# Optimization experiments

Hardware: AMD Instinct MI355X
Metric: run time of the kernel (lower is better)

## Reference

```python
import jax, jax.numpy as jnp
import numpy as np

DIM = 512
HEADS = 8
DHEAD = 64
WIN = 128
QK_SCALE = 8.0
LN_EPS = 1e-5


def setup_inputs() -> dict:
    key = jax.random.key(0)
    ks = jax.random.split(key, 5)
    B, N = 8, 4096
    x = jax.random.normal(ks[0], (B, N, DIM), jnp.float32)
    w_qkv = jax.random.normal(ks[1], (3 * HEADS * DHEAD, DIM), jnp.float32) * 0.02
    w_out = jax.random.normal(ks[2], (DIM, HEADS * DHEAD), jnp.float32) * 0.02
    b_out = jnp.zeros((DIM,), jnp.float32)
    w_ff1 = jax.random.normal(ks[3], (4 * DIM, DIM), jnp.float32) * 0.02
    w_ff2 = jax.random.normal(ks[4], (DIM, 4 * DIM), jnp.float32) * 0.02
    return {
        'x': x, 'w_qkv': w_qkv,
        'q_scale': jnp.ones((DHEAD,), jnp.float32),
        'k_scale': jnp.ones((DHEAD,), jnp.float32),
        'w_out': w_out, 'b_out': b_out,
        'ln1_g': jnp.ones((DIM,), jnp.float32), 'ln1_b': jnp.zeros((DIM,), jnp.float32),
        'ff_ln_g': jnp.ones((DIM,), jnp.float32), 'ff_ln_b': jnp.zeros((DIM,), jnp.float32),
        'w_ff1': w_ff1, 'w_ff2': w_ff2,
    }


def _ln(x, g, b):
    m = jnp.mean(x, axis=-1, keepdims=True)
    v = jnp.mean((x - m) ** 2, axis=-1, keepdims=True)
    return (x - m) * jax.lax.rsqrt(v + LN_EPS) * g + b


def _l2norm(t):
    return t / jnp.clip(jnp.linalg.norm(t, axis=-1, keepdims=True), 1e-12)


def _rotary(t, pos):
    # t: (B, H, N, DHEAD); standard (non-xpos) rotary, half-split style
    inv_freq = 1.0 / (10000.0 ** (jnp.arange(0, DHEAD, 2, dtype=jnp.float32) / DHEAD))
    freqs = pos[:, None] * inv_freq                      # (N, DHEAD/2)
    emb = jnp.concatenate([freqs, freqs], axis=-1)       # (N, DHEAD)
    cos, sin = jnp.cos(emb), jnp.sin(emb)
    t1, t2 = t[..., : DHEAD // 2], t[..., DHEAD // 2:]
    rot = jnp.concatenate([-t2, t1], axis=-1)
    return t * cos + rot * sin


def reference(x, w_qkv, q_scale, k_scale, w_out, b_out, ln1_g, ln1_b,
              ff_ln_g, ff_ln_b, w_ff1, w_ff2):
    B, N, D = x.shape
    nw = N // WIN

    # ---- LocalMHA (prenorm, qk-rmsnorm, sliding window, causal) ----
    h = _ln(x, ln1_g, ln1_b)
    qkv = h @ w_qkv.T                                    # (B, N, 3*H*DHEAD)
    q, k, v = jnp.split(qkv, 3, axis=-1)

    def to_heads(t):
        return t.reshape(B, N, HEADS, DHEAD).transpose(0, 2, 1, 3)  # (B,H,N,d)

    q, k, v = to_heads(q), to_heads(k), to_heads(v)
    q = _l2norm(q) * q_scale
    k = _l2norm(k) * k_scale
    pos = jnp.arange(N, dtype=jnp.float32)
    q = _rotary(q, pos)
    k = _rotary(k, pos)

    # bucket into windows; keys/values look back one window
    bq = q.reshape(B, HEADS, nw, WIN, DHEAD)
    bk = k.reshape(B, HEADS, nw, WIN, DHEAD)
    bv = v.reshape(B, HEADS, nw, WIN, DHEAD)

    def look_back(t):
        prev = jnp.concatenate([jnp.zeros_like(t[:, :, :1]), t[:, :, :-1]], axis=2)
        return jnp.concatenate([prev, t], axis=3)

    kk, vv = look_back(bk), look_back(bv)

    qpos = jnp.arange(N, dtype=jnp.int32).reshape(nw, WIN)
    kprev = jnp.concatenate([jnp.full((1, WIN), -1, jnp.int32), qpos[:-1]], axis=0)
    kpos = jnp.concatenate([kprev, qpos], axis=1)
    mask = (qpos[:, :, None] >= kpos[:, None, :]) & (kpos[:, None, :] >= 0)

    sim = jnp.einsum('bhnid,bhnjd->bhnij', bq, kk) * QK_SCALE
    sim = jnp.where(mask, sim, -1e9)
    attn = jax.nn.softmax(sim, axis=-1)
    out = jnp.einsum('bhnij,bhnjd->bhnid', attn, vv)
    out = out.reshape(B, HEADS, N, DHEAD).transpose(0, 2, 1, 3).reshape(B, N, HEADS * DHEAD)
    x = x + out @ w_out.T + b_out

    # ---- FeedForward: LN -> Linear(4D, no bias) -> GELU -> Linear(D, no bias) ----
    hf = _ln(x, ff_ln_g, ff_ln_b)
    ff = jax.nn.gelu(hf @ w_ff1.T, approximate=False) @ w_ff2.T
    return x + ff
```

## Files before the change

kernel.cpp:

```cpp
#include <hip/hip_runtime.h>
#include <cstdint>
#include <cstddef>

typedef __bf16 bf16;
typedef __bf16 bf16x8 __attribute__((ext_vector_type(8)));
typedef float f32x4 __attribute__((ext_vector_type(4)));

#define DEV static __device__ __forceinline__

constexpr int BATCH = 8;
constexpr int SEQ = 4096;
constexpr int DIM = 512;
constexpr int HEADS = 8;
constexpr int DH = 64;
constexpr int WIN = 128;
constexpr int NW = SEQ / WIN;
constexpr int TOK = BATCH * SEQ;
constexpr float EPS = 1e-5f;

constexpr size_t R_EL   = (size_t)TOK * DIM;
constexpr size_t C_QKV  = 0;
constexpr size_t C_WOUT = 786432;
constexpr size_t C_WF1  = 1048576;
constexpr size_t C_WF2  = 2097152;
constexpr size_t C_SM   = 3145728;
constexpr size_t P_EL   = 3148416;

DEV void gload_lds16(const void* g, void* l) {
  __builtin_amdgcn_global_load_lds((__attribute__((address_space(1))) void*)g,
                                   (__attribute__((address_space(3))) void*)l,
                                   16, 0, 0);
}

DEV f32x4 mfma16(bf16x8 a, bf16x8 b, f32x4 c) {
  return __builtin_amdgcn_mfma_f32_16x16x32_bf16(a, b, c, 0, 0, 0);
}

DEV float fast_gelu(float v) {
  const float z = fabsf(v) * 0.7071067811865476f;
  const float t = __builtin_amdgcn_rcpf(1.0f + 0.3275911f * z);
  const float p = t * (0.254829592f +
                  t * (-0.284496736f +
                  t * (1.421413741f +
                  t * (-1.453152027f +
                  t * 1.061405429f))));
  const float e = __expf(-z * z);
  const float erfa = 1.0f - p * e;
  const float cdf = 0.5f + copysignf(0.5f * erfa, v);
  return v * cdf;
}

struct SrcPtrs { const void* p[12]; };

DEV void copy8(const void* src, long si, bf16* dst, bool f32) {
  if (f32) {
    const float4* s = (const float4*)((const float*)src + si);
    float4 a = s[0], b = s[1];
    bf16x8 o;
    o[0] = (bf16)a.x; o[1] = (bf16)a.y; o[2] = (bf16)a.z; o[3] = (bf16)a.w;
    o[4] = (bf16)b.x; o[5] = (bf16)b.y; o[6] = (bf16)b.z; o[7] = (bf16)b.w;
    *(bf16x8*)dst = o;
  } else {
    *(bf16x8*)dst = *(const bf16x8*)((const bf16*)src + si);
  }
}

__global__ __launch_bounds__(256) void ingest_kernel(SrcPtrs sp, bf16* cano) {
  const bool f32 = (((const unsigned short*)sp.p[2])[0] == 0);
  const long e = (long)threadIdx.x * 8;
  int b = blockIdx.x;
  if (b < 384)  { long o = (long)b * 2048 + e; copy8(sp.p[1], o, cano + C_QKV + o, f32); return; }
  b -= 384;
  if (b < 128)  { long o = (long)b * 2048 + e; copy8(sp.p[4], o, cano + C_WOUT + o, f32); return; }
  b -= 128;
  if (b < 512)  { long o = (long)b * 2048 + e; copy8(sp.p[10], o, cano + C_WF1 + o, f32); return; }
  b -= 512;
  if (b < 512)  { long o = (long)b * 2048 + e; copy8(sp.p[11], o, cano + C_WF2 + o, f32); return; }
  b -= 512;
  const long o = (long)b * 2048 + e;
  if (o >= 2688) return;
  const void* src; long si;
  if      (o < 64)   { src = sp.p[2]; si = o; }
  else if (o < 128)  { src = sp.p[3]; si = o - 64; }
  else if (o < 640)  { src = sp.p[5]; si = o - 128; }
  else if (o < 1152) { src = sp.p[6]; si = o - 640; }
  else if (o < 1664) { src = sp.p[7]; si = o - 1152; }
  else if (o < 2176) { src = sp.p[8]; si = o - 1664; }
  else               { src = sp.p[9]; si = o - 2176; }
  copy8(src, si, cano + C_SM + o, f32);
}

__global__ __launch_bounds__(256) void ln_kernel(const void* __restrict__ in,
                                                 const bf16* __restrict__ gg,
                                                 const bf16* __restrict__ bb,
                                                 bf16* __restrict__ out,
                                                 const unsigned short* __restrict__ probe,
                                                 int raw) {
  const int wave = threadIdx.x >> 6, lane = threadIdx.x & 63;
  const int row = blockIdx.x * 4 + wave;
  const size_t base = (size_t)row * DIM + lane * 8;
  float f[8];
  if (raw && probe[0] == 0) {
    const float4* p = (const float4*)((const float*)in + base);
    float4 a = p[0], bq = p[1];
    f[0] = a.x; f[1] = a.y; f[2] = a.z; f[3] = a.w;
    f[4] = bq.x; f[5] = bq.y; f[6] = bq.z; f[7] = bq.w;
  } else {
    bf16x8 v = *(const bf16x8*)((const bf16*)in + base);
#pragma unroll
    for (int i = 0; i < 8; ++i) f[i] = (float)v[i];
  }
  float s = 0.f, sq = 0.f;
#pragma unroll
  for (int i = 0; i < 8; ++i) { s += f[i]; sq += f[i] * f[i]; }
#pragma unroll
  for (int m = 32; m; m >>= 1) { s += __shfl_xor(s, m); sq += __shfl_xor(sq, m); }
  const float mean = s * (1.0f / DIM);
  const float var = fmaxf(sq * (1.0f / DIM) - mean * mean, 0.0f);
  const float rs = rsqrtf(var + EPS);
  bf16x8 gv = *(const bf16x8*)(gg + lane * 8);
  bf16x8 bv = *(const bf16x8*)(bb + lane * 8);
  bf16x8 o;
#pragma unroll
  for (int i = 0; i < 8; ++i) o[i] = (bf16)((f[i] - mean) * rs * (float)gv[i] + (float)bv[i]);
  *(bf16x8*)((bf16*)out + base) = o;
}

template <int MODE>
__global__ __launch_bounds__(512) void gemm_bt(const bf16* __restrict__ A,
                                               const bf16* __restrict__ Bw,
                                               bf16* __restrict__ O0, bf16* __restrict__ O1,
                                               bf16* __restrict__ O2,
                                               float* __restrict__ Of,
                                               const void* __restrict__ Xraw,
                                               const bf16* __restrict__ Xb,
                                               const bf16* __restrict__ bias,
                                               const unsigned short* __restrict__ probe,
                                               int K, int bstride, int ostride, int gx) {
  extern __shared__ __align__(16) bf16 smem[];
  const int tid = threadIdx.x;
  const int wid = tid >> 6, lane = tid & 63;
  const int l15 = lane & 15, quad = lane >> 4;
  const int id = blockIdx.x;
  const int per = gx * 8;
  const int tM = ((id / per) * 8 + (id & 7)) * 256;
  const int tN = ((id % per) >> 3) * 128;
  const int wM = (wid >> 1) * 64, wN = (wid & 1) * 64;
  const int kq = (quad ^ ((l15 >> 1) & 3)) * 8;
  f32x4 acc[4][4];
  const f32x4 z = {0.f, 0.f, 0.f, 0.f};
#pragma unroll
  for (int i = 0; i < 4; ++i)
#pragma unroll
    for (int j = 0; j < 4; ++j) acc[i][j] = z;

  const int cA0 = tid,       rA0 = cA0 >> 2, sA0 = (((cA0 & 3) ^ ((cA0 >> 3) & 3)) * 8);
  const int cA1 = tid + 512, rA1 = cA1 >> 2, sA1 = (((cA1 & 3) ^ ((cA1 >> 3) & 3)) * 8);
  const int cB0 = tid,       rB0 = cB0 >> 2, sB0 = sA0;

  auto stage = [&](int t, int p) {
    const int k0 = t * 32;
    bf16* dA = smem + p * 12288;
    bf16* dB = dA + 8192;
    gload_lds16(A  + (size_t)(tM + rA0) * K       + k0 + sA0, &dA[cA0 * 8]);
    gload_lds16(A  + (size_t)(tM + rA1) * K       + k0 + sA1, &dA[cA1 * 8]);
    gload_lds16(Bw + (size_t)(tN + rB0) * bstride + k0 + sB0, &dB[cB0 * 8]);
  };

  const int nt = K >> 5;
  stage(0, 0);
  stage(1, 1);
  __builtin_amdgcn_sched_barrier(0);
  asm volatile("s_waitcnt vmcnt(3)" ::: "memory");
  __builtin_amdgcn_s_barrier();
  __builtin_amdgcn_sched_barrier(0);

  int cur = 0;
  for (int t = 0; t < nt; ++t) {
    if (t + 2 < nt) {
      int nx = cur + 2; if (nx >= 3) nx -= 3;
      stage(t + 2, nx);
    }
    const bf16* As = smem + cur * 12288;
    const bf16* Bs = As + 8192;
    bf16x8 aF[4], bF[4];
#pragma unroll
    for (int i = 0; i < 4; ++i) aF[i] = *(const bf16x8*)&As[(wM + i * 16 + l15) * 32 + kq];
#pragma unroll
    for (int j = 0; j < 4; ++j) bF[j] = *(const bf16x8*)&Bs[(wN + j * 16 + l15) * 32 + kq];
#pragma unroll
    for (int i = 0; i < 4; ++i)
#pragma unroll
      for (int j = 0; j < 4; ++j) acc[i][j] = mfma16(aF[i], bF[j], acc[i][j]);
    if (t < nt - 1) {
      __builtin_amdgcn_sched_barrier(0);
      if (t + 2 < nt) asm volatile("s_waitcnt vmcnt(3)" ::: "memory");
      else            asm volatile("s_waitcnt vmcnt(0)" ::: "memory");
      __builtin_amdgcn_s_barrier();
      __builtin_amdgcn_sched_barrier(0);
    }
    ++cur; if (cur == 3) cur = 0;
  }
  const int q0 = nt % 3;
  bf16* eb = smem + q0 * 12288;

  if constexpr (MODE == 0) {
    bf16* ob = eb + wid * 1152;
    const int colbase = tN + wN;
    const int which = colbase >> 9;
    const int head = (colbase >> 6) & 7;
    bf16* dst = which == 0 ? O0 : (which == 1 ? O1 : O2);
    const int ch = lane & 7;
    float scv[8], invf[8];
    if (which < 2) {
      const bf16* sc = which ? bias : Xb;
      bf16x8 s8 = *(const bf16x8*)(sc + ch * 8);
#pragma unroll
      for (int u = 0; u < 8; ++u) {
        scv[u] = (float)s8[u] * (which == 0 ? 8.0f : 1.0f);
        invf[u] = exp2f(-(float)((ch & 3) * 8 + u) * (13.287712379549449f / 32.0f));
      }
    }
#pragma unroll
    for (int i = 0; i < 4; ++i) {
#pragma unroll
      for (int j = 0; j < 4; ++j)
#pragma unroll
        for (int r = 0; r < 4; ++r)
          ob[(quad * 4 + r) * 72 + j * 16 + l15] = (bf16)acc[i][j][r];
#pragma unroll
      for (int t = 0; t < 2; ++t) {
        const int rr = t * 8 + (lane >> 3);
        const int rowg = tM + wM + i * 16 + rr;
        bf16x8 ov = *(const bf16x8*)&ob[rr * 72 + ch * 8];
        float f[8];
#pragma unroll
        for (int u = 0; u < 8; ++u) f[u] = (float)ov[u];
        if (which < 2) {
          float ss = 0.f;
#pragma unroll
          for (int u = 0; u < 8; ++u) ss += f[u] * f[u];
          ss += __shfl_xor(ss, 1); ss += __shfl_xor(ss, 2); ss += __shfl_xor(ss, 4);
          const float rs = 1.0f / fmaxf(sqrtf(ss), 1e-12f);
#pragma unroll
          for (int u = 0; u < 8; ++u) f[u] *= rs * scv[u];
          float pf[8];
#pragma unroll
          for (int u = 0; u < 8; ++u) pf[u] = __shfl_xor(f[u], 4);
          const float pos = (float)(rowg & (SEQ - 1));
#pragma unroll
          for (int u = 0; u < 8; ++u) {
            float sn, cs;
            __sincosf(pos * invf[u], &sn, &cs);
            const float rot = (ch < 4) ? -pf[u] : pf[u];
            f[u] = f[u] * cs + rot * sn;
          }
        }
        bf16x8 o8;
#pragma unroll
        for (int u = 0; u < 8; ++u) o8[u] = (bf16)f[u];
        const int bb = rowg >> 12, n = rowg & (SEQ - 1);
        *(bf16x8*)(dst + ((size_t)(bb * HEADS + head) * SEQ + n) * DH + ch * 8) = o8;
      }
    }
    return;
  }

  if constexpr (MODE == 1) {
    bf16* ob = eb + wid * 1152;
    const int ch = lane & 7;
    bf16x8 bias8 = *(const bf16x8*)(bias + tN + wN + ch * 8);
    const bool xf32 = (probe[0] == 0);
#pragma unroll
    for (int i = 0; i < 4; ++i) {
#pragma unroll
      for (int j = 0; j < 4; ++j)
#pragma unroll
        for (int r = 0; r < 4; ++r)
          ob[(quad * 4 + r) * 72 + j * 16 + l15] = (bf16)acc[i][j][r];
#pragma unroll
      for (int t = 0; t < 2; ++t) {
        const int rr = t * 8 + (lane >> 3);
        const int rowg = tM + wM + i * 16 + rr;
        bf16x8 ov = *(const bf16x8*)&ob[rr * 72 + ch * 8];
        bf16x8 o8;
        const size_t idx = (size_t)rowg * DIM + tN + wN + ch * 8;
        float xr[8];
        if (xf32) {
          const float4* xp = (const float4*)((const float*)Xraw + idx);
          float4 a = xp[0], bq = xp[1];
          xr[0] = a.x; xr[1] = a.y; xr[2] = a.z; xr[3] = a.w;
          xr[4] = bq.x; xr[5] = bq.y; xr[6] = bq.z; xr[7] = bq.w;
        } else {
          bf16x8 xv = *(const bf16x8*)((const bf16*)Xraw + idx);
#pragma unroll
          for (int u = 0; u < 8; ++u) xr[u] = (float)xv[u];
        }
#pragma unroll
        for (int u = 0; u < 8; ++u) o8[u] = (bf16)((float)ov[u] + xr[u] + (float)bias8[u]);
        *(bf16x8*)(O0 + idx) = o8;
      }
    }
    return;
  }
}

__global__ __launch_bounds__(512, 2) void ffn_fused(const bf16* __restrict__ hf,
                                                    const bf16* __restrict__ W1,
                                                    const bf16* __restrict__ W2,
                                                    const bf16* __restrict__ x2,
                                                    float* __restrict__ out) {
  extern __shared__ __align__(16) bf16 smem[];
  const int tid = threadIdx.x;
  const int wid = tid >> 6, lane = tid & 63;
  const int l15 = lane & 15, quad = lane >> 4;
  const int tM = blockIdx.x * 128;
  const int wM  = (wid >> 2) * 64;
  const int wN1 = (wid & 3) * 32;
  const int wN2 = (wid & 3) * 128;
  const int kq = (quad ^ ((l15 >> 1) & 3)) * 8;
  bf16* f1c = smem + 24576;

  const int srow = tid >> 2;
  const int scol = ((tid & 3) ^ ((tid >> 3) & 3)) * 8;

  auto stage1 = [&](int cc, int t, int p) {
    const int k0 = t * 32;
    bf16* dH = smem + p * 8192;
    bf16* dW = dH + 4096;
    gload_lds16(hf + (size_t)(tM + srow) * DIM + k0 + scol, &dH[tid * 8]);
    gload_lds16(W1 + (size_t)(cc * 128 + srow) * DIM + k0 + scol, &dW[tid * 8]);
  };

  f32x4 acc2[4][8];
  const f32x4 z = {0.f, 0.f, 0.f, 0.f};
#pragma unroll
  for (int i = 0; i < 4; ++i)
#pragma unroll
    for (int j = 0; j < 8; ++j) acc2[i][j] = z;

  stage1(0, 0, 0);
  stage1(0, 1, 1);
  __builtin_amdgcn_sched_barrier(0);
  asm volatile("s_waitcnt vmcnt(2)" ::: "memory");
  __builtin_amdgcn_s_barrier();
  __builtin_amdgcn_sched_barrier(0);

  for (int c = 0; c < 16; ++c) {
    f32x4 acc1[4][2];
#pragma unroll
    for (int i = 0; i < 4; ++i) { acc1[i][0] = z; acc1[i][1] = z; }
    int cur = 0;
    for (int t = 0; t < 16; ++t) {
      if (t + 2 < 16) {
        int nx = cur + 2; if (nx >= 3) nx -= 3;
        stage1(c, t + 2, nx);
      }
      const bf16* Hs = smem + cur * 8192;
      const bf16* Ws = Hs + 4096;
      bf16x8 aF[4], bF[2];
#pragma unroll
      for (int i = 0; i < 4; ++i) aF[i] = *(const bf16x8*)&Hs[(wM + i * 16 + l15) * 32 + kq];
#pragma unroll
      for (int j = 0; j < 2; ++j) bF[j] = *(const bf16x8*)&Ws[(wN1 + j * 16 + l15) * 32 + kq];
#pragma unroll
      for (int i = 0; i < 4; ++i)
#pragma unroll
        for (int j = 0; j < 2; ++j) acc1[i][j] = mfma16(aF[i], bF[j], acc1[i][j]);
      if (t < 15) {
        __builtin_amdgcn_sched_barrier(0);
        if (t + 2 < 16) asm volatile("s_waitcnt vmcnt(2)" ::: "memory");
        else            asm volatile("s_waitcnt vmcnt(0)" ::: "memory");
        __builtin_amdgcn_s_barrier();
        __builtin_amdgcn_sched_barrier(0);
      }
      ++cur; if (cur == 3) cur = 0;
    }
    __builtin_amdgcn_sched_barrier(0);
    __builtin_amdgcn_s_barrier();
    __builtin_amdgcn_sched_barrier(0);
#pragma unroll
    for (int i = 0; i < 4; ++i)
#pragma unroll
      for (int j = 0; j < 2; ++j)
#pragma unroll
        for (int r = 0; r < 4; ++r) {
          const int rowW = wM + i * 16 + quad * 4 + r;
          const int colW = wN1 + j * 16 + l15;
          f1c[rowW * 128 + ((((colW >> 3) ^ (rowW & 7))) << 3) + (colW & 7)] =
              (bf16)fast_gelu(acc1[i][j][r]);
        }
    if (c < 15) { stage1(c + 1, 0, 0); stage1(c + 1, 1, 1); }
    asm volatile("s_waitcnt lgkmcnt(0)" ::: "memory");
    __builtin_amdgcn_sched_barrier(0);
    __builtin_amdgcn_s_barrier();
    __builtin_amdgcn_sched_barrier(0);
    const bf16* w2c = W2 + c * 128;
#pragma unroll
    for (int kk = 0; kk < 4; ++kk) {
      bf16x8 a2[4], b2[8];
#pragma unroll
      for (int i = 0; i < 4; ++i) {
        const int row = wM + i * 16 + l15;
        a2[i] = *(const bf16x8*)&f1c[row * 128 + (((kk * 4 + quad) ^ (l15 & 7)) << 3)];
      }
#pragma unroll
      for (int j = 0; j < 8; ++j)
        b2[j] = *(const bf16x8*)(w2c + (size_t)(wN2 + j * 16 + l15) * 2048 + kk * 32 + quad * 8);
#pragma unroll
      for (int i = 0; i < 4; ++i)
#pragma unroll
        for (int j = 0; j < 8; ++j) acc2[i][j] = mfma16(a2[i], b2[j], acc2[i][j]);
    }
    if (c < 15) {
      __builtin_amdgcn_sched_barrier(0);
      asm volatile("s_waitcnt vmcnt(2)" ::: "memory");
      __builtin_amdgcn_s_barrier();
      __builtin_amdgcn_sched_barrier(0);
    }
  }

  __builtin_amdgcn_sched_barrier(0);
  __builtin_amdgcn_s_barrier();
  __builtin_amdgcn_sched_barrier(0);
  float* obf = (float*)f1c + wid * 1024;
  const int ch = lane & 7;
#pragma unroll
  for (int i = 0; i < 4; ++i)
#pragma unroll
    for (int jh = 0; jh < 2; ++jh) {
#pragma unroll
      for (int j2 = 0; j2 < 4; ++j2)
#pragma unroll
        for (int r = 0; r < 4; ++r)
          obf[(quad * 4 + r) * 64 + j2 * 16 + l15] = acc2[i][jh * 4 + j2][r];
#pragma unroll
      for (int t = 0; t < 2; ++t) {
        const int rr = t * 8 + (lane >> 3);
        const int rowg = tM + wM + i * 16 + rr;
        const size_t idx = (size_t)rowg * DIM + wN2 + jh * 64 + ch * 8;
        const float4* rp = (const float4*)&obf[rr * 64 + ch * 8];
        float4 a = rp[0], b = rp[1];
        float f[8] = {a.x, a.y, a.z, a.w, b.x, b.y, b.z, b.w};
        bf16x8 xv = *(const bf16x8*)(x2 + idx);
#pragma unroll
        for (int u = 0; u < 8; ++u) f[u] += (float)xv[u];
        float4 o0 = {f[0], f[1], f[2], f[3]}, o1 = {f[4], f[5], f[6], f[7]};
        ((float4*)(out + idx))[0] = o0;
        ((float4*)(out + idx))[1] = o1;
      }
    }
}

__global__ __launch_bounds__(256, 3) void attn_kernel(const bf16* __restrict__ q,
                                                      const bf16* __restrict__ k,
                                                      const bf16* __restrict__ v,
                                                      bf16* __restrict__ ao) {
  __shared__ __align__(16) bf16 kv[256 * 72];
  __shared__ __align__(16) bf16 pbuf[4][16 * 136];
  const int w = blockIdx.x, h = blockIdx.y, b = blockIdx.z;
  const int tid = threadIdx.x;
  const int wv = tid >> 6, lane = tid & 63;
  const int l15 = lane & 15, quad = lane >> 4;
  const size_t bh = (size_t)b * HEADS + h;
  const bf16* qb = q + bh * SEQ * DH;
  const bf16* kb = k + bh * SEQ * DH;
  const bf16* vb = v + bh * SEQ * DH;
  const int t0 = (w - 1) * WIN;

#pragma unroll
  for (int it = 0; it < 8; ++it) {
    const int c = it * 256 + tid;
    const int tok = c >> 3, ch = c & 7;
    int gt = t0 + tok; gt = gt < 0 ? 0 : gt;
    *(bf16x8*)&kv[tok * 72 + ch * 8] = *(const bf16x8*)(kb + (size_t)gt * DH + ch * 8);
  }
  bf16x8 aQ[2][2];
#pragma unroll
  for (int qt = 0; qt < 2; ++qt) {
    const int qtok = w * WIN + wv * 32 + qt * 16 + l15;
#pragma unroll
    for (int ks = 0; ks < 2; ++ks)
      aQ[qt][ks] = *(const bf16x8*)(qb + (size_t)qtok * DH + ks * 32 + quad * 8);
  }
  int gtv = t0 + tid; gtv = gtv < 0 ? 0 : gtv;
  bf16x8 vld[8];
#pragma unroll
  for (int dg = 0; dg < 8; ++dg)
    vld[dg] = *(const bf16x8*)(vb + (size_t)gtv * DH + dg * 8);
  __syncthreads();

  bf16x8 aP[2][8];
#pragma unroll
  for (int qt = 0; qt < 2; ++qt) {
    f32x4 sreg[16];
#pragma unroll
    for (int nt = 0; nt < 16; ++nt) {
      f32x4 a = {0.f, 0.f, 0.f, 0.f};
#pragma unroll
      for (int ks = 0; ks < 2; ++ks) {
        bf16x8 bK = *(const bf16x8*)&kv[(nt * 16 + l15) * 72 + ks * 32 + quad * 8];
        a = mfma16(aQ[qt][ks], bK, a);
      }
      sreg[nt] = a;
    }
    const int qlb = wv * 32 + qt * 16 + quad * 4;
    float rinv[4];
#pragma unroll
    for (int r = 0; r < 4; ++r) {
      const int ql = qlb + r;
      float sum = 0.f;
#pragma unroll
      for (int nt = 0; nt < 16; ++nt) {
        const int j = nt * 16 + l15;
        const bool valid = (nt < 8) ? (w > 0) : (ql >= j - WIN);
        const float p = valid ? __expf(sreg[nt][r]) : 0.0f;
        sreg[nt][r] = p;
        sum += p;
      }
#pragma unroll
      for (int m = 8; m; m >>= 1) sum += __shfl_xor(sum, m);
      rinv[r] = 1.0f / sum;
    }
#pragma unroll
    for (int half = 0; half < 2; ++half) {
#pragma unroll
      for (int ntw = 0; ntw < 8; ++ntw)
#pragma unroll
        for (int r = 0; r < 4; ++r)
          pbuf[wv][(quad * 4 + r) * 136 + ntw * 16 + l15] =
              (bf16)(sreg[half * 8 + ntw][r] * rinv[r]);
#pragma unroll
      for (int kk = 0; kk < 4; ++kk)
        aP[qt][half * 4 + kk] = *(const bf16x8*)&pbuf[wv][l15 * 136 + kk * 32 + quad * 8];
    }
  }
  __syncthreads();

#pragma unroll
  for (int dg = 0; dg < 8; ++dg)
#pragma unroll
    for (int i = 0; i < 8; ++i)
      kv[(dg * 8 + i) * 264 + tid] = vld[dg][i];
  __syncthreads();

#pragma unroll
  for (int qt = 0; qt < 2; ++qt) {
#pragma unroll
    for (int dt = 0; dt < 4; ++dt) {
      f32x4 o = {0.f, 0.f, 0.f, 0.f};
#pragma unroll
      for (int ks2 = 0; ks2 < 8; ++ks2) {
        bf16x8 bV = *(const bf16x8*)&kv[(dt * 16 + l15) * 264 + ks2 * 32 + quad * 8];
        o = mfma16(aP[qt][ks2], bV, o);
      }
#pragma unroll
      for (int r = 0; r < 4; ++r)
        pbuf[wv][(quad * 4 + r) * 136 + dt * 16 + l15] = (bf16)o[r];
    }
#pragma unroll
    for (int t = 0; t < 2; ++t) {
      const int rr = t * 8 + (lane >> 3), ch = lane & 7;
      bf16x8 ov = *(const bf16x8*)&pbuf[wv][rr * 136 + ch * 8];
      const int tok = w * WIN + wv * 32 + qt * 16 + rr;
      *(bf16x8*)(ao + ((size_t)b * SEQ + tok) * DIM + h * DH + ch * 8) = ov;
    }
  }
}

extern "C" void kernel_launch(void* const* d_in, const int* in_sizes, int n_in,
                              void* d_out, int out_size, void* d_ws, size_t ws_size,
                              hipStream_t stream) {
  (void)in_sizes; (void)n_in; (void)out_size; (void)ws_size;
  float* out = (float*)d_out;
  bf16* cano = (bf16*)d_ws;
  const unsigned short* probe = (const unsigned short*)d_in[2];

  SrcPtrs sp;
  for (int i = 0; i < 12; ++i) sp.p[i] = d_in[i];

  bf16* slot0 = cano + P_EL;
  bf16* slot1 = cano + P_EL + R_EL;
  bf16* slot2 = cano + P_EL + 2 * R_EL;
  bf16* slot3 = cano + P_EL + 3 * R_EL;

  const bf16* qsc  = cano + C_SM + 0;
  const bf16* ksc  = cano + C_SM + 64;
  const bf16* bout = cano + C_SM + 128;
  const bf16* l1g  = cano + C_SM + 640;
  const bf16* l1b  = cano + C_SM + 1152;
  const bf16* lfg  = cano + C_SM + 1664;
  const bf16* lfb  = cano + C_SM + 2176;

  constexpr int LDSB = 3 * 12288 * 2;
  constexpr int LDSF = 81920;
  static bool attr_done = false;
  if (!attr_done) {
    hipFuncSetAttribute((const void*)gemm_bt<0>, hipFuncAttributeMaxDynamicSharedMemorySize, LDSB);
    hipFuncSetAttribute((const void*)gemm_bt<1>, hipFuncAttributeMaxDynamicSharedMemorySize, LDSB);
    hipFuncSetAttribute((const void*)ffn_fused, hipFuncAttributeMaxDynamicSharedMemorySize, LDSF);
    attr_done = true;
  }

  ingest_kernel<<<1538, 256, 0, stream>>>(sp, cano);
  ln_kernel<<<TOK / 4, 256, 0, stream>>>(d_in[0], l1g, l1b, slot0, probe, 1);
  gemm_bt<0><<<16 * 96, 512, LDSB, stream>>>(slot0, cano + C_QKV, slot1, slot2, slot3,
                                             nullptr, nullptr, qsc, ksc, probe,
                                             DIM, DIM, 0, 12);
  attn_kernel<<<dim3(NW, HEADS, BATCH), 256, 0, stream>>>(slot1, slot2, slot3, slot0);
  gemm_bt<1><<<16 * 32, 512, LDSB, stream>>>(slot0, cano + C_WOUT, slot1, nullptr, nullptr,
                                             nullptr, d_in[0], nullptr, bout, probe,
                                             DIM, DIM, 0, 4);
  ln_kernel<<<TOK / 4, 256, 0, stream>>>(slot1, lfg, lfb, slot0, probe, 0);
  ffn_fused<<<TOK / 128, 512, LDSF, stream>>>(slot0, cano + C_WF1, cano + C_WF2,
                                              slot1, out);
}
```

Before: 552.6 us.

## Restructure fused FFN: 64-row tiles, resident LN input, pipelined W2 loads

The fused FFN kernel now processes 64-row tiles instead of 128, doubling the grid to 512 blocks, and loads the whole 64x512 normalized input tile into LDS once rather than restreaming it for each of the 16 hidden chunks. Only W1 goes through the three-slot ring, with one continuous pipeline across chunk boundaries. W2 fragments are double-buffered in registers so the next k-slice loads while MFMAs run, and block ids are swizzled into the row mapping. LDS per block grows to about 104KB, which likely limits occupancy to one block per CU, and each weight byte is reused across half as many rows.

After: 676.5 us. +22.4%, slower.

```diff
diff --git a/kernel.cpp b/kernel.cpp
--- a/kernel.cpp
+++ b/kernel.cpp
@@ -311,110 +311,116 @@
                                                     const bf16* __restrict__ x2,
                                                     float* __restrict__ out) {
   extern __shared__ __align__(16) bf16 smem[];
+  bf16* hfs  = smem;
+  bf16* ring = smem + 32768;
+  bf16* f1c  = smem + 45056;
   const int tid = threadIdx.x;
   const int wid = tid >> 6, lane = tid & 63;
   const int l15 = lane & 15, quad = lane >> 4;
-  const int tM = blockIdx.x * 128;
-  const int wM  = (wid >> 2) * 64;
-  const int wN1 = (wid & 3) * 32;
-  const int wN2 = (wid & 3) * 128;
-  const int kq = (quad ^ ((l15 >> 1) & 3)) * 8;
-  bf16* f1c = smem + 24576;
-
-  const int srow = tid >> 2;
-  const int scol = ((tid & 3) ^ ((tid >> 3) & 3)) * 8;
-
-  auto stage1 = [&](int cc, int t, int p) {
-    const int k0 = t * 32;
-    bf16* dH = smem + p * 8192;
-    bf16* dW = dH + 4096;
-    gload_lds16(hf + (size_t)(tM + srow) * DIM + k0 + scol, &dH[tid * 8]);
-    gload_lds16(W1 + (size_t)(cc * 128 + srow) * DIM + k0 + scol, &dW[tid * 8]);
+  const int id = blockIdx.x;
+  const int tM = ((id & 7) * 64 + (id >> 3)) * 64;
+  const int wm = (wid >> 2) * 32;
+  const int wn1 = (wid & 3) * 32;
+  const int wn2 = (wid & 3) * 128;
+  const int mA = l15 & 7;
+  const int mB = (l15 >> 1) & 3;
+
+#pragma unroll
+  for (int it = 0; it < 8; ++it) {
+    const int c0 = it * 512 + tid;
+    const int row = c0 >> 6, slot = c0 & 63;
+    const int g = slot ^ (row & 7);
+    gload_lds16(hf + (size_t)(tM + row) * 512 + g * 8, hfs + c0 * 8);
+  }
+  const int rrow = tid >> 2;
+  const int rg = ((tid & 3) ^ ((tid >> 3) & 3)) * 8;
+  auto stageW1 = [&](int T) {
+    const int c = T >> 4, t = T & 15, p = T % 3;
+    gload_lds16(W1 + (size_t)(c * 128 + rrow) * 512 + t * 32 + rg,
+                ring + p * 4096 + tid * 8);
   };
-
-  f32x4 acc2[4][8];
-  const f32x4 z = {0.f, 0.f, 0.f, 0.f};
-#pragma unroll
-  for (int i = 0; i < 4; ++i)
-#pragma unroll
-    for (int j = 0; j < 8; ++j) acc2[i][j] = z;
-
-  stage1(0, 0, 0);
-  stage1(0, 1, 1);
+  stageW1(0); stageW1(1);
   __builtin_amdgcn_sched_barrier(0);
-  asm volatile("s_waitcnt vmcnt(2)" ::: "memory");
+  asm volatile("s_waitcnt vmcnt(1)" ::: "memory");
   __builtin_amdgcn_s_barrier();
   __builtin_amdgcn_sched_barrier(0);
 
+  f32x4 acc2[2][8];
+  const f32x4 z = {0.f, 0.f, 0.f, 0.f};
+#pragma unroll
+  for (int i = 0; i < 2; ++i)
+#pragma unroll
+    for (int j = 0; j < 8; ++j) acc2[i][j] = z;
+  bf16x8 b2a[8], b2b[8];
+
   for (int c = 0; c < 16; ++c) {
-    f32x4 acc1[4][2];
-#pragma unroll
-    for (int i = 0; i < 4; ++i) { acc1[i][0] = z; acc1[i][1] = z; }
-    int cur = 0;
+    f32x4 acc1[2][2];
+    acc1[0][0] = z; acc1[0][1] = z; acc1[1][0] = z; acc1[1][1] = z;
     for (int t = 0; t < 16; ++t) {
-      if (t + 2 < 16) {
-        int nx = cur + 2; if (nx >= 3) nx -= 3;
-        stage1(c, t + 2, nx);
-      }
-      const bf16* Hs = smem + cur * 8192;
-      const bf16* Ws = Hs + 4096;
-      bf16x8 aF[4], bF[2];
-#pragma unroll
-      for (int i = 0; i < 4; ++i) aF[i] = *(const bf16x8*)&Hs[(wM + i * 16 + l15) * 32 + kq];
-#pragma unroll
-      for (int j = 0; j < 2; ++j) bF[j] = *(const bf16x8*)&Ws[(wN1 + j * 16 + l15) * 32 + kq];
-#pragma unroll
-      for (int i = 0; i < 4; ++i)
+      const int T = c * 16 + t;
+      if (T + 2 < 256) stageW1(T + 2);
+      const bf16* rgp = ring + (T % 3) * 4096;
+      bf16x8 aF[2], bF[2];
+#pragma unroll
+      for (int i = 0; i < 2; ++i)
+        aF[i] = *(const bf16x8*)&hfs[(wm + i * 16 + l15) * 512 + ((t * 4 + quad) ^ mA) * 8];
+#pragma unroll
+      for (int j = 0; j < 2; ++j)
+        bF[j] = *(const bf16x8*)&rgp[(wn1 + j * 16 + l15) * 32 + (quad ^ mB) * 8];
+#pragma unroll
+      for (int i = 0; i < 2; ++i)
 #pragma unroll
         for (int j = 0; j < 2; ++j) acc1[i][j] = mfma16(aF[i], bF[j], acc1[i][j]);
       if (t < 15) {
         __builtin_amdgcn_sched_barrier(0);
-        if (t + 2 < 16) asm volatile("s_waitcnt vmcnt(2)" ::: "memory");
-        else            asm volatile("s_waitcnt vmcnt(0)" ::: "memory");
+        if (T + 2 < 256) asm volatile("s_waitcnt vmcnt(1)" ::: "memory");
+        else             asm volatile("s_waitcnt vmcnt(0)" ::: "memory");
         __builtin_amdgcn_s_barrier();
         __builtin_amdgcn_sched_barrier(0);
       }
-      ++cur; if (cur == 3) cur = 0;
-    }
-    __builtin_amdgcn_sched_barrier(0);
-    __builtin_amdgcn_s_barrier();
-    __builtin_amdgcn_sched_barrier(0);
-#pragma unroll
-    for (int i = 0; i < 4; ++i)
+    }
+    const bf16* w2c = W2 + c * 128;
+#pragma unroll
+    for (int i = 0; i < 2; ++i)
 #pragma unroll
       for (int j = 0; j < 2; ++j)
 #pragma unroll
         for (int r = 0; r < 4; ++r) {
-          const int rowW = wM + i * 16 + quad * 4 + r;
-          const int colW = wN1 + j * 16 + l15;
-          f1c[rowW * 128 + ((((colW >> 3) ^ (rowW & 7))) << 3) + (colW & 7)] =
+          const int rw = wm + i * 16 + quad * 4 + r;
+          const int cw = wn1 + j * 16 + l15;
+          f1c[rw * 128 + (((cw >> 3) ^ (rw & 7)) << 3) + (cw & 7)] =
               (bf16)fast_gelu(acc1[i][j][r]);
         }
-    if (c < 15) { stage1(c + 1, 0, 0); stage1(c + 1, 1, 1); }
+#pragma unroll
+    for (int j = 0; j < 8; ++j)
+      b2a[j] = *(const bf16x8*)(w2c + (size_t)(wn2 + j * 16 + l15) * 2048 + quad * 8);
     asm volatile("s_waitcnt lgkmcnt(0)" ::: "memory");
     __builtin_amdgcn_sched_barrier(0);
     __builtin_amdgcn_s_barrier();
     __builtin_amdgcn_sched_barrier(0);
-    const bf16* w2c = W2 + c * 128;
 #pragma unroll
     for (int kk = 0; kk < 4; ++kk) {
-      bf16x8 a2[4], b2[8];
-#pragma unroll
-      for (int i = 0; i < 4; ++i) {
-        const int row = wM + i * 16 + l15;
-        a2[i] = *(const bf16x8*)&f1c[row * 128 + (((kk * 4 + quad) ^ (l15 & 7)) << 3)];
-      }
-#pragma unroll
-      for (int j = 0; j < 8; ++j)
-        b2[j] = *(const bf16x8*)(w2c + (size_t)(wN2 + j * 16 + l15) * 2048 + kk * 32 + quad * 8);
-#pragma unroll
-      for (int i = 0; i < 4; ++i)
-#pragma unroll
-        for (int j = 0; j < 8; ++j) acc2[i][j] = mfma16(a2[i], b2[j], acc2[i][j]);
+      if (kk < 3) {
+#pragma unroll
+        for (int j = 0; j < 8; ++j) {
+          bf16x8 v = *(const bf16x8*)(w2c + (size_t)(wn2 + j * 16 + l15) * 2048 +
+                                      (kk + 1) * 32 + quad * 8);
+          if (kk & 1) b2a[j] = v; else b2b[j] = v;
+        }
+      }
+      bf16x8 a2[2];
+#pragma unroll
+      for (int i = 0; i < 2; ++i)
+        a2[i] = *(const bf16x8*)&f1c[(wm + i * 16 + l15) * 128 + ((kk * 4 + quad) ^ mA) * 8];
+#pragma unroll
+      for (int i = 0; i < 2; ++i)
+#pragma unroll
+        for (int j = 0; j < 8; ++j)
+          acc2[i][j] = mfma16(a2[i], (kk & 1) ? b2b[j] : b2a[j], acc2[i][j]);
     }
     if (c < 15) {
       __builtin_amdgcn_sched_barrier(0);
-      asm volatile("s_waitcnt vmcnt(2)" ::: "memory");
+      asm volatile("s_waitcnt vmcnt(1)" ::: "memory");
       __builtin_amdgcn_s_barrier();
       __builtin_amdgcn_sched_barrier(0);
     }
@@ -423,23 +429,23 @@
   __builtin_amdgcn_sched_barrier(0);
   __builtin_amdgcn_s_barrier();
   __builtin_amdgcn_sched_barrier(0);
-  float* obf = (float*)f1c + wid * 1024;
-  const int ch = lane & 7;
-#pragma unroll
-  for (int i = 0; i < 4; ++i)
-#pragma unroll
-    for (int jh = 0; jh < 2; ++jh) {
-#pragma unroll
-      for (int j2 = 0; j2 < 4; ++j2)
-#pragma unroll
-        for (int r = 0; r < 4; ++r)
-          obf[(quad * 4 + r) * 64 + j2 * 16 + l15] = acc2[i][jh * 4 + j2][r];
-#pragma unroll
-      for (int t = 0; t < 2; ++t) {
+  float* obf = (float*)smem + wid * 2048;
+#pragma unroll
+  for (int i = 0; i < 2; ++i) {
+#pragma unroll
+    for (int j = 0; j < 8; ++j)
+#pragma unroll
+      for (int r = 0; r < 4; ++r)
+        obf[(quad * 4 + r) * 128 + j * 16 + l15] = acc2[i][j][r];
+#pragma unroll
+    for (int t = 0; t < 2; ++t)
+#pragma unroll
+      for (int cp = 0; cp < 2; ++cp) {
         const int rr = t * 8 + (lane >> 3);
-        const int rowg = tM + wM + i * 16 + rr;
-        const size_t idx = (size_t)rowg * DIM + wN2 + jh * 64 + ch * 8;
-        const float4* rp = (const float4*)&obf[rr * 64 + ch * 8];
+        const int col = cp * 64 + (lane & 7) * 8;
+        const int rowg = tM + wm + i * 16 + rr;
+        const size_t idx = (size_t)rowg * DIM + wn2 + col;
+        const float4* rp = (const float4*)&obf[rr * 128 + col];
         float4 a = rp[0], b = rp[1];
         float f[8] = {a.x, a.y, a.z, a.w, b.x, b.y, b.z, b.w};
         bf16x8 xv = *(const bf16x8*)(x2 + idx);
@@ -449,7 +455,7 @@
         ((float4*)(out + idx))[0] = o0;
         ((float4*)(out + idx))[1] = o1;
       }
-    }
+  }
 }
 
 __global__ __launch_bounds__(256, 3) void attn_kernel(const bf16* __restrict__ q,
@@ -593,7 +599,7 @@
   const bf16* lfb  = cano + C_SM + 2176;
 
   constexpr int LDSB = 3 * 12288 * 2;
-  constexpr int LDSF = 81920;
+  constexpr int LDSF = 53248 * 2;
   static bool attr_done = false;
   if (!attr_done) {
     hipFuncSetAttribute((const void*)gemm_bt<0>, hipFuncAttributeMaxDynamicSharedMemorySize, LDSB);
@@ -612,6 +618,5 @@
                                              nullptr, d_in[0], nullptr, bout, probe,
                                              DIM, DIM, 0, 4);
   ln_kernel<<<TOK / 4, 256, 0, stream>>>(slot1, lfg, lfb, slot0, probe, 0);
-  ffn_fused<<<TOK / 128, 512, LDSF, stream>>>(slot0, cano + C_WF1, cano + C_WF2,
-                                              slot1, out);
-}
+  ffn_fused<<<512, 512, LDSF, stream>>>(slot0, cano + C_WF1, cano + C_WF2, slot1, out);
+}
```
